# Kernel optimization log

Hardware: AMD Instinct MI355X
Metric: run time of the kernel (lower is better)

Reference implementation:

```python
import jax, jax.numpy as jnp
import numpy as np

BATCH = 16
MAX_SEQLEN = 8192
D_MODEL = 1024
TOTAL = 65536  # sum of sequence lengths


def setup_inputs() -> dict:
    key = jax.random.key(0)
    k_buf, _ = jax.random.split(key)
    # Position buffer (e.g. precomputed position embeddings), first dim >= max length.
    buffer = jax.random.normal(k_buf, (MAX_SEQLEN, D_MODEL), dtype=jnp.float32)
    # Build ragged offsets: BATCH lengths, each <= MAX_SEQLEN, summing to TOTAL.
    rng = np.random.default_rng(0)
    base = TOTAL // BATCH  # 4096
    d = rng.integers(0, 2048, size=BATCH // 2)
    lengths = np.concatenate([base + d, base - d])
    rng.shuffle(lengths)
    offsets = jnp.asarray(np.concatenate([[0], np.cumsum(lengths)]), dtype=jnp.int32)
    return {"buffer": buffer, "offsets": offsets, "total_tokens": TOTAL}


def reference(buffer, offsets, total_tokens):
    # Equivalent of: for each sequence i with length L_i = offsets[i+1]-offsets[i],
    # take buffer[:L_i]; concatenate into jagged values sharing the same offsets.
    # Done in one vectorized pass: local position of each flat token = idx - offsets[seg].
    idx = jnp.arange(total_tokens, dtype=jnp.int32)                      # [T]
    seg = jnp.searchsorted(offsets, idx, side="right") - 1              # [T] sequence id
    pos = idx - offsets[seg]                                             # [T] ragged arange
    values = buffer[pos]                                                 # [T, D] jagged values
    return values
```

## Files before the change

### kernel.cpp

```cpp
#include <hip/hip_runtime.h>


#define D_MODEL 1024
#define V4 (D_MODEL / 4)
#define ROWS_PER_BLOCK 32
#define UNROLL 8
#define MAX_OFF 64

typedef float v4f __attribute__((ext_vector_type(4)));

__global__ __launch_bounds__(256, 8) void positionid_gather(
    const v4f* __restrict__ buf,
    const int* __restrict__ offsets,
    int n_off,
    v4f*       __restrict__ out,
    int T)
{
    __shared__ int soff[MAX_OFF];
    const int tid = threadIdx.x;
    if (tid < n_off) soff[tid] = offsets[tid];
    __syncthreads();

    const int t0 = blockIdx.x * ROWS_PER_BLOCK;
    if (t0 >= T) return;

    int seg = 0;
    while (seg + 2 < n_off && soff[seg + 1] <= t0) ++seg;

    if (t0 + ROWS_PER_BLOCK <= T) {
        for (int r = 0; r < ROWS_PER_BLOCK; r += UNROLL) {
            int pos[UNROLL];
            #pragma unroll
            for (int k = 0; k < UNROLL; ++k) {
                const int t = t0 + r + k;
                while (seg + 2 < n_off && soff[seg + 1] <= t) ++seg;
                pos[k] = t - soff[seg];
            }
            v4f v[UNROLL];
            #pragma unroll
            for (int k = 0; k < UNROLL; ++k)
                v[k] = buf[(size_t)pos[k] * V4 + tid];
            #pragma unroll
            for (int k = 0; k < UNROLL; ++k)
                __builtin_nontemporal_store(
                    v[k], &out[(size_t)(t0 + r + k) * V4 + tid]);
        }
    } else {
        for (int r = 0; r < ROWS_PER_BLOCK; ++r) {
            const int t = t0 + r;
            if (t >= T) break;
            while (seg + 2 < n_off && soff[seg + 1] <= t) ++seg;
            const int pos = t - soff[seg];
            v4f v = buf[(size_t)pos * V4 + tid];
            __builtin_nontemporal_store(v, &out[(size_t)t * V4 + tid]);
        }
    }
}

extern "C" void kernel_launch(void* const* d_in, const int* in_sizes, int n_in,
                              void* d_out, int out_size, void* d_ws, size_t ws_size,
                              hipStream_t stream) {
    const v4f* buf     = (const v4f*)d_in[0];
    const int* offsets = (const int*)d_in[1];
    const int  n_off   = in_sizes[1];
    v4f*       out     = (v4f*)d_out;

    const int T = out_size / D_MODEL;

    const int nblocks = (T + ROWS_PER_BLOCK - 1) / ROWS_PER_BLOCK;
    positionid_gather<<<dim3(nblocks), dim3(256), 0, stream>>>(
        buf, offsets, n_off, out, T);
}
```

Before: 309.9 us.

## Replace per-token gather with per-position scatter reusing each buffer row across segments

Inverts the loop order: each block loads a few buffer rows once and writes them to every sequence whose length exceeds that position. This cuts global reads of the buffer from one per output token to one per buffer row and drops the per-token segment search. In exchange, blocks for high positions do little work, so load is uneven, and the grid now depends on buffer rows rather than total tokens. Output rows past the buffer length are never written, so correctness relies on every sequence length being at most the buffer size.

```diff
diff --git a/kernel.cpp b/kernel.cpp
--- a/kernel.cpp
+++ b/kernel.cpp
@@ -3,56 +3,43 @@
 
 #define D_MODEL 1024
 #define V4 (D_MODEL / 4)
-#define ROWS_PER_BLOCK 32
-#define UNROLL 8
+#define RPOS 4
 #define MAX_OFF 64
 
 typedef float v4f __attribute__((ext_vector_type(4)));
 
-__global__ __launch_bounds__(256, 8) void positionid_gather(
+__global__ __launch_bounds__(256, 8) void positionid_scatter(
     const v4f* __restrict__ buf,
     const int* __restrict__ offsets,
     int n_off,
     v4f*       __restrict__ out,
-    int T)
+    int buf_rows)
 {
     __shared__ int soff[MAX_OFF];
     const int tid = threadIdx.x;
     if (tid < n_off) soff[tid] = offsets[tid];
     __syncthreads();
 
-    const int t0 = blockIdx.x * ROWS_PER_BLOCK;
-    if (t0 >= T) return;
+    const int p0 = blockIdx.x * RPOS;
+    if (p0 >= buf_rows) return;
 
-    int seg = 0;
-    while (seg + 2 < n_off && soff[seg + 1] <= t0) ++seg;
+    v4f v[RPOS];
+    #pragma unroll
+    for (int k = 0; k < RPOS; ++k) {
+        const int p = p0 + k;
+        v[k] = buf[(size_t)(p < buf_rows ? p : 0) * V4 + tid];
+    }
 
-    if (t0 + ROWS_PER_BLOCK <= T) {
-        for (int r = 0; r < ROWS_PER_BLOCK; r += UNROLL) {
-            int pos[UNROLL];
-            #pragma unroll
-            for (int k = 0; k < UNROLL; ++k) {
-                const int t = t0 + r + k;
-                while (seg + 2 < n_off && soff[seg + 1] <= t) ++seg;
-                pos[k] = t - soff[seg];
-            }
-            v4f v[UNROLL];
-            #pragma unroll
-            for (int k = 0; k < UNROLL; ++k)
-                v[k] = buf[(size_t)pos[k] * V4 + tid];
-            #pragma unroll
-            for (int k = 0; k < UNROLL; ++k)
+    const int nseg = n_off - 1;
+    for (int i = 0; i < nseg; ++i) {
+        const int base = soff[i];
+        const int len  = soff[i + 1] - base;
+        #pragma unroll
+        for (int k = 0; k < RPOS; ++k) {
+            const int p = p0 + k;
+            if (p < len)
                 __builtin_nontemporal_store(
-                    v[k], &out[(size_t)(t0 + r + k) * V4 + tid]);
-        }
-    } else {
-        for (int r = 0; r < ROWS_PER_BLOCK; ++r) {
-            const int t = t0 + r;
-            if (t >= T) break;
-            while (seg + 2 < n_off && soff[seg + 1] <= t) ++seg;
-            const int pos = t - soff[seg];
-            v4f v = buf[(size_t)pos * V4 + tid];
-            __builtin_nontemporal_store(v, &out[(size_t)t * V4 + tid]);
+                    v[k], &out[(size_t)(base + p) * V4 + tid]);
         }
     }
 }
@@ -65,9 +52,9 @@
     const int  n_off   = in_sizes[1];
     v4f*       out     = (v4f*)d_out;
 
-    const int T = out_size / D_MODEL;
+    const int buf_rows = in_sizes[0] / D_MODEL;
 
-    const int nblocks = (T + ROWS_PER_BLOCK - 1) / ROWS_PER_BLOCK;
-    positionid_gather<<<dim3(nblocks), dim3(256), 0, stream>>>(
-        buf, offsets, n_off, out, T);
+    const int nblocks = (buf_rows + RPOS - 1) / RPOS;
+    positionid_scatter<<<dim3(nblocks), dim3(256), 0, stream>>>(
+        buf, offsets, n_off, out, buf_rows);
 }
```

Result: faster. 295.0 us (-4.8%).
